# Kernel optimization log

Measured on AMD Instinct MI355X. Metric: run time of the kernel, lower is better.

## Reference

```python
import jax, jax.numpy as jnp
import numpy as np

K = 8  # 2^3 kernel offsets for kernel-size-2, stride-2 transposed conv in 3D (HYPER_CUBE)
HID = 64


def sp_convT(x, W, parent, kofs):
    """Sparse generative transposed conv via kernel map.
    x: [Nin, Cin]; W: [K, Cin, Cout]; parent: [Nout] int; kofs: [Nout] int in [0,K).
    out[j] = x[parent[j]] @ W[kofs[j]].
    """
    xg = x[parent]  # [Nout, Cin] gather
    out = jnp.zeros((parent.shape[0], W.shape[2]), dtype=x.dtype)
    for k in range(K):  # fixed small structural loop over kernel offsets
        out = out + jnp.where((kofs == k)[:, None], xg @ W[k], jnp.zeros((), x.dtype))
    return out


def setup_inputs() -> dict:
    key = jax.random.key(0)
    ks = jax.random.split(key, 12)
    Ns = [5000, 20000, 80000, 320000]
    sc_i = 1.0 / np.sqrt(64)
    inp = {
        'x0': jax.random.normal(ks[0], (Ns[0], 64), jnp.float32),
        'x1': jax.random.normal(ks[1], (Ns[1], 64), jnp.float32),
        'x2': jax.random.normal(ks[2], (Ns[2], 64), jnp.float32),
        'W_i': jax.random.normal(ks[3], (K, 64, 4 * HID), jnp.float32) * sc_i,
        'W_h': jax.random.normal(ks[4], (K, HID, 4 * HID), jnp.float32) * sc_i,
        'W_c': jax.random.normal(ks[5], (K, HID, HID), jnp.float32) * sc_i,
        'parent0': jax.random.randint(ks[6], (Ns[1],), 0, Ns[0], jnp.int32),
        'kofs0': jax.random.randint(ks[7], (Ns[1],), 0, K, jnp.int32),
        'parent1': jax.random.randint(ks[8], (Ns[2],), 0, Ns[1], jnp.int32),
        'kofs1': jax.random.randint(ks[9], (Ns[2],), 0, K, jnp.int32),
        'parent2': jax.random.randint(ks[10], (Ns[3],), 0, Ns[2], jnp.int32),
        'kofs2': jax.random.randint(ks[11], (Ns[3],), 0, K, jnp.int32),
    }
    return inp


def reference(x0, x1, x2, W_i, W_h, W_c, parent0, kofs0, parent1, kofs1, parent2, kofs2):
    xs = [x0, x1, x2]
    parents = [parent0, parent1, parent2]
    kofss = [kofs0, kofs1, kofs2]
    hx = jnp.zeros((x0.shape[0], HID), dtype=x0.dtype)
    cx = jnp.zeros((x0.shape[0], HID), dtype=x0.dtype)
    for t in range(3):  # coder_num timesteps (structural loop)
        p, ko = parents[t], kofss[t]
        cx = sp_convT(cx, W_c, p, ko)                                   # upsample cell state
        gates = sp_convT(hx, W_h, p, ko) + sp_convT(xs[t], W_i, p, ko)  # [Nout, 4*HID]
        in_g, fg, cg, og = jnp.split(gates, 4, axis=1)
        in_g = jax.nn.sigmoid(in_g)
        fg = jax.nn.sigmoid(fg)
        cg = jax.nn.sigmoid(cg)  # NOTE: original uses sigmoid (not tanh) for cell_gate
        og = jax.nn.sigmoid(og)
        cx = fg * cx + in_g * cg
        hx = og * jnp.tanh(cx)
    return hx
```

## Files before the change

### kernel.cpp

```cpp
#include <hip/hip_runtime.h>


#define KNUM 8
#define TM 32
#define STEP_THREADS 256

typedef __attribute__((ext_vector_type(8))) _Float16 f16x8;
typedef __attribute__((ext_vector_type(4))) float f32x4;

__device__ __forceinline__ float fsig(float x) {
  return __builtin_amdgcn_rcpf(1.0f + __expf(-x));
}
__device__ __forceinline__ float ftanh_(float x) {
  float e = __expf(2.0f * x);
  return 1.0f - 2.0f * __builtin_amdgcn_rcpf(e + 1.0f);
}
__device__ __forceinline__ f16x8 to_h8(float4 a, float4 b) {
  f16x8 r;
  r[0] = (_Float16)a.x; r[1] = (_Float16)a.y; r[2] = (_Float16)a.z; r[3] = (_Float16)a.w;
  r[4] = (_Float16)b.x; r[5] = (_Float16)b.y; r[6] = (_Float16)b.z; r[7] = (_Float16)b.w;
  return r;
}

__global__ void prep_w_kernel(const float* __restrict__ Wi, const float* __restrict__ Wh,
                              const float* __restrict__ Wc,
                              _Float16* __restrict__ WgT, _Float16* __restrict__ WcT) {
  int tid = blockIdx.x * blockDim.x + threadIdx.x;
  int stride = gridDim.x * blockDim.x;
  for (int idx = tid; idx < KNUM * 256 * 128; idx += stride) {
    int k  = idx >> 15;
    int co = (idx >> 7) & 255;
    int ci = idx & 127;
    float v = (ci < 64) ? Wh[(k * 64 + ci) * 256 + co]
                        : Wi[(k * 64 + ci - 64) * 256 + co];
    WgT[idx] = (_Float16)v;
  }
  for (int idx = tid; idx < KNUM * 64 * 64; idx += stride) {
    int k  = idx >> 12;
    int co = (idx >> 6) & 63;
    int ci = idx & 63;
    WcT[idx] = (_Float16)Wc[(k * 64 + ci) * 64 + co];
  }
}

__device__ __forceinline__ void seg_select(int b, int& seg, int& rb, int& nb) {
  if (b < 32)       { seg = 0; rb = b;       nb = 32;  }
  else if (b < 160) { seg = 1; rb = b - 32;  nb = 128; }
  else              { seg = 2; rb = b - 160; nb = 352; }
}

__global__ void scatter_all_kernel(const int* __restrict__ k0, const int* __restrict__ p0, int n0,
                                   int2* __restrict__ op0, int cap0,
                                   const int* __restrict__ k1, const int* __restrict__ p1, int n1,
                                   int2* __restrict__ op1, int cap1,
                                   const int* __restrict__ k2, const int* __restrict__ p2, int n2,
                                   int2* __restrict__ op2, int cap2,
                                   int* __restrict__ cursor) {
  int seg, rb, nb;
  seg_select(blockIdx.x, seg, rb, nb);
  const int* kp = seg == 0 ? k0 : seg == 1 ? k1 : k2;
  const int* pp = seg == 0 ? p0 : seg == 1 ? p1 : p2;
  int n   = seg == 0 ? n0 : seg == 1 ? n1 : n2;
  int cap = seg == 0 ? cap0 : seg == 1 ? cap1 : cap2;
  int2* op = seg == 0 ? op0 : seg == 1 ? op1 : op2;
  int* cur = cursor + seg * KNUM;

  __shared__ int h[KNUM], base[KNUM];
  if (threadIdx.x < KNUM) h[threadIdx.x] = 0;
  __syncthreads();
  int chunk = (n + nb - 1) / nb;
  int c0 = rb * chunk;
  int c1 = min(n, c0 + chunk);
  for (int i = c0 + threadIdx.x; i < c1; i += blockDim.x)
    atomicAdd(&h[kp[i]], 1);
  __syncthreads();
  if (threadIdx.x < KNUM) {
    base[threadIdx.x] = h[threadIdx.x] ? atomicAdd(&cur[threadIdx.x], h[threadIdx.x]) : 0;
    h[threadIdx.x] = 0;
  }
  __syncthreads();
  for (int i = c0 + threadIdx.x; i < c1; i += blockDim.x) {
    int k = kp[i];
    int rel = base[k] + atomicAdd(&h[k], 1);
    op[k * cap + rel] = make_int2(i, pp[i]);
  }
}

template <bool FIRST, bool LAST>
__global__ __launch_bounds__(STEP_THREADS)
void lstm_step_kernel(const float* __restrict__ xf32, const _Float16* __restrict__ hc_in,
                      const int2* __restrict__ op, const int* __restrict__ counts, int cap,
                      const _Float16* __restrict__ WgT, const _Float16* __restrict__ WcT,
                      float* __restrict__ out32, _Float16* __restrict__ hc_out, int bpk) {
  __shared__ __align__(16) _Float16 A[TM][136];
  __shared__ __align__(16) _Float16 Cg[TM][72];
  __shared__ int jidx[TM];
  __shared__ __align__(16) char Obuf[9216];
  float (*O32)[68] = (float(*)[68])Obuf;
  _Float16 (*Oh)[72] = (_Float16(*)[72])Obuf;
  _Float16 (*Oc)[72] = (_Float16(*)[72])(Obuf + 32 * 72 * 2);

  const int kb = blockIdx.x & 7;
  const int bi = blockIdx.x >> 3;
  const int cnt = counts[kb];
  const int off = kb * cap;
  const int ntiles = (cnt + TM - 1) / TM;
  if (bi >= ntiles || cnt == 0) return;

  const int tid  = threadIdx.x;
  const int lane = tid & 63;
  const int wcq  = tid >> 6;
  const int l15  = lane & 15;
  const int kg   = lane >> 4;

  f16x8 bg[4][4];
  f16x8 bc[2];
  {
    const _Float16* wgp = WgT + (size_t)kb * (256 * 128);
#pragma unroll
    for (int g = 0; g < 4; ++g)
#pragma unroll
      for (int ks = (FIRST ? 2 : 0); ks < 4; ++ks)
        bg[g][ks] = *(const f16x8*)(wgp + (size_t)(64 * g + 16 * wcq + l15) * 128 + ks * 32 + kg * 8);
    if constexpr (!FIRST) {
      const _Float16* wcp = WcT + (size_t)kb * (64 * 64);
#pragma unroll
      for (int ks = 0; ks < 2; ++ks)
        bc[ks] = *(const f16x8*)(wcp + (size_t)(16 * wcq + l15) * 64 + ks * 32 + kg * 8);
    }
  }

  const int gr  = tid >> 3;
  const int gq8 = tid & 7;

  auto ld_jp = [&](int tt) -> int2 {
    int grow = tt * TM + gr;
    bool v = (tt < ntiles) && (grow < cnt);
    int2 jp = op[off + min(grow, cnt - 1)];
    if (!v) jp.x = -1;
    return jp;
  };

  float4 xA0{}, xA1{}; f16x8 hA{}, cA{}; int jA = -1;
  float4 xB0{}, xB1{}; f16x8 hB{}, cB{}; int jB = -1;
  int2 jpP;

  auto rows_into = [&](int2 jp, float4& rx0, float4& rx1, f16x8& rh, f16x8& rc, int& rj) {
    int p = jp.y;
    const float4* xr = (const float4*)(xf32 + (size_t)p * 64 + gq8 * 8);
    rx0 = xr[0]; rx1 = xr[1];
    if constexpr (!FIRST) {
      const _Float16* hr = hc_in + (size_t)p * 128 + gq8 * 8;
      rh = *(const f16x8*)(hr);
      rc = *(const f16x8*)(hr + 64);
    }
    rj = jp.x;
  };

  rows_into(ld_jp(bi), xA0, xA1, hA, cA, jA);
  rows_into(ld_jp(bi + bpk), xB0, xB1, hB, cB, jB);
  jpP = ld_jp(bi + 2 * bpk);

#define HALF_STEP(TCUR, RX0, RX1, RH, RC, RJ)                                   \
  {                                                                             \
    asm volatile("s_barrier" ::: "memory");         \
    if (gq8 == 0) jidx[gr] = RJ;                                                \
    *(f16x8*)&A[gr][64 + gq8 * 8] = to_h8(RX0, RX1);                            \
    if constexpr (!FIRST) {                                                     \
      *(f16x8*)&A[gr][gq8 * 8]  = RH;                                           \
      *(f16x8*)&Cg[gr][gq8 * 8] = RC;                                           \
    }                                                                           \
    asm volatile("s_waitcnt lgkmcnt(0)\n\ts_barrier" ::: "memory");             \
    rows_into(jpP, RX0, RX1, RH, RC, RJ);         \
    jpP = ld_jp((TCUR) + 3 * bpk);                                              \
    f32x4 aG[2][4];                                                             \
    f32x4 aC[2];                                                                \
    _Pragma("unroll")                                                           \
    for (int rf = 0; rf < 2; ++rf) {                                            \
      _Pragma("unroll")                                                         \
      for (int g = 0; g < 4; ++g) aG[rf][g] = f32x4{0.f, 0.f, 0.f, 0.f};        \
      aC[rf] = f32x4{0.f, 0.f, 0.f, 0.f};                                       \
    }                                                                           \
    _Pragma("unroll")                                                           \
    for (int ks = (FIRST ? 2 : 0); ks < 4; ++ks) {                              \
      _Pragma("unroll")                                                         \
      for (int rf = 0; rf < 2; ++rf) {                                          \
        f16x8 a = *(const f16x8*)&A[16 * rf + l15][ks * 32 + kg * 8];           \
        aG[rf][0] = __builtin_amdgcn_mfma_f32_16x16x32_f16(a, bg[0][ks], aG[rf][0], 0, 0, 0); \
        aG[rf][1] = __builtin_amdgcn_mfma_f32_16x16x32_f16(a, bg[1][ks], aG[rf][1], 0, 0, 0); \
        aG[rf][2] = __builtin_amdgcn_mfma_f32_16x16x32_f16(a, bg[2][ks], aG[rf][2], 0, 0, 0); \
        aG[rf][3] = __builtin_amdgcn_mfma_f32_16x16x32_f16(a, bg[3][ks], aG[rf][3], 0, 0, 0); \
      }                                                                         \
    }                                                                           \
    if constexpr (!FIRST) {                                                     \
      _Pragma("unroll")                                                         \
      for (int ks = 0; ks < 2; ++ks) {                                          \
        _Pragma("unroll")                                                       \
        for (int rf = 0; rf < 2; ++rf) {                                        \
          f16x8 a = *(const f16x8*)&Cg[16 * rf + l15][ks * 32 + kg * 8];        \
          aC[rf] = __builtin_amdgcn_mfma_f32_16x16x32_f16(a, bc[ks], aC[rf], 0, 0, 0); \
        }                                                                       \
      }                                                                         \
    }                                                                           \
                                                  \
    _Pragma("unroll")                                                           \
    for (int rf = 0; rf < 2; ++rf) {                                            \
      _Pragma("unroll")                                                         \
      for (int r = 0; r < 4; ++r) {                                             \
        int row = 16 * rf + kg * 4 + r;           \
        float ing = fsig(aG[rf][0][r]);                                         \
        float fg  = fsig(aG[rf][1][r]);                                         \
        float cgt = fsig(aG[rf][2][r]);       \
        float og  = fsig(aG[rf][3][r]);                                         \
        float cup = FIRST ? 0.0f : aC[rf][r];                                   \
        float cxv = fg * cup + ing * cgt;                                       \
        float hxv = og * ftanh_(cxv);                                           \
        int ch = 16 * wcq + l15;                                                \
        if constexpr (LAST) {                                                   \
          O32[row][ch] = hxv;                                                   \
        } else {                                                                \
          Oh[row][ch] = (_Float16)hxv;                                          \
          Oc[row][ch] = (_Float16)cxv;                                          \
        }                                                                       \
      }                                                                         \
    }                                                                           \
    asm volatile("s_waitcnt lgkmcnt(0)\n\ts_barrier" ::: "memory");             \
                 \
    {                                                                           \
      int srow = tid >> 3, sc = tid & 7;                                        \
      int j = jidx[srow];                                                       \
      if (j >= 0) {                                                             \
        if constexpr (LAST) {                                                   \
          f32x4 v0 = *(const f32x4*)&O32[srow][sc * 8];                         \
          f32x4 v1 = *(const f32x4*)&O32[srow][sc * 8 + 4];                     \
          float* dst = out32 + (size_t)j * 64 + sc * 8;                         \
          *(f32x4*)dst = v0;                                                    \
          *(f32x4*)(dst + 4) = v1;                                              \
        } else {                                                                \
          f16x8 vh = *(const f16x8*)&Oh[srow][sc * 8];                          \
          f16x8 vc = *(const f16x8*)&Oc[srow][sc * 8];                          \
          _Float16* dst = hc_out + (size_t)j * 128 + sc * 8;                    \
          *(f16x8*)dst = vh;                                                    \
          *(f16x8*)(dst + 64) = vc;                                             \
        }                                                                       \
      }                                                                         \
    }                                                                           \
  }

  for (int t = bi; t < ntiles; t += 2 * bpk) {
    HALF_STEP(t, xA0, xA1, hA, cA, jA);
    if (t + bpk < ntiles) {
      HALF_STEP(t + bpk, xB0, xB1, hB, cB, jB);
    }
  }
#undef HALF_STEP
}

static inline int idiv_up(int a, int b) { return (a + b - 1) / b; }

template <bool FIRST, bool LAST>
static void run_step(const float* xf32, const _Float16* hc_in,
                     const int2* op, int nout, const int* counts, int cap,
                     const _Float16* WgT, const _Float16* WcT,
                     float* out32, _Float16* hc_out, hipStream_t stream) {
  int bpk = idiv_up(nout, KNUM * TM);
  if (bpk > 160) bpk = 160;
  if (bpk < 1) bpk = 1;
  lstm_step_kernel<FIRST, LAST><<<dim3(KNUM * bpk), dim3(STEP_THREADS), 0, stream>>>(
      xf32, hc_in, op, counts, cap, WgT, WcT, out32, hc_out, bpk);
}

extern "C" void kernel_launch(void* const* d_in, const int* in_sizes, int n_in,
                              void* d_out, int out_size, void* d_ws, size_t ws_size,
                              hipStream_t stream) {
  const float* x0 = (const float*)d_in[0];
  const float* x1 = (const float*)d_in[1];
  const float* x2 = (const float*)d_in[2];
  const float* Wi = (const float*)d_in[3];
  const float* Wh = (const float*)d_in[4];
  const float* Wc = (const float*)d_in[5];
  const int* parent0 = (const int*)d_in[6];
  const int* kofs0   = (const int*)d_in[7];
  const int* parent1 = (const int*)d_in[8];
  const int* kofs1   = (const int*)d_in[9];
  const int* parent2 = (const int*)d_in[10];
  const int* kofs2   = (const int*)d_in[11];
  const int N1 = in_sizes[6];
  const int N2 = in_sizes[8];
  const int N3 = in_sizes[10];

  const int cap0 = idiv_up(N1, KNUM) + N1 / 32 + 256;
  const int cap1 = idiv_up(N2, KNUM) + N2 / 32 + 256;
  const int cap2 = idiv_up(N3, KNUM) + N3 / 32 + 256;

  char* w = (char*)d_ws;
  auto carve = [&](size_t bytes) {
    char* p = w;
    w += (bytes + 255) & ~(size_t)255;
    return p;
  };
  _Float16* WgT = (_Float16*)carve((size_t)KNUM * 256 * 128 * 2);
  _Float16* WcT = (_Float16*)carve((size_t)KNUM * 64 * 64 * 2);
  int* cursor   = (int*)carve(3 * KNUM * sizeof(int));
  int2* op0     = (int2*)carve((size_t)KNUM * cap0 * sizeof(int2));
  int2* op1     = (int2*)carve((size_t)KNUM * cap1 * sizeof(int2));
  int2* op2     = (int2*)carve((size_t)KNUM * cap2 * sizeof(int2));
  _Float16* hc_a = (_Float16*)carve((size_t)N1 * 128 * 2);
  _Float16* hc_b = (_Float16*)carve((size_t)N2 * 128 * 2);
  (void)ws_size; (void)n_in; (void)out_size;

  hipMemsetAsync(cursor, 0, 3 * KNUM * sizeof(int), stream);
  prep_w_kernel<<<256, 256, 0, stream>>>(Wi, Wh, Wc, WgT, WcT);
  scatter_all_kernel<<<512, 256, 0, stream>>>(kofs0, parent0, N1, op0, cap0,
                                              kofs1, parent1, N2, op1, cap1,
                                              kofs2, parent2, N3, op2, cap2,
                                              cursor);

  run_step<true, false>(x0, nullptr, op0, N1, cursor + 0 * KNUM, cap0,
                        WgT, WcT, nullptr, hc_a, stream);
  run_step<false, false>(x1, hc_a, op1, N2, cursor + 1 * KNUM, cap1,
                         WgT, WcT, nullptr, hc_b, stream);
  run_step<false, true>(x2, hc_b, op2, N3, cursor + 2 * KNUM, cap2,
                        WgT, WcT, (float*)d_out, nullptr, stream);
}
```

Measured before the change: 104.8 us.

## Pack next-step x into fp16 state rows and rewrite scatter with wave ballots

Each LSTM step now reads the next timestep's x row, indexed by the output row, converts it to fp16 and stores it beside h and c in a 192-wide state row. The next step then gathers h, c and x with one contiguous fp16 read per parent instead of a separate fp32 random gather of x. The scatter kernel switches from a strided loop with shared-memory atomics to one element per thread, ranked within each wavefront by ballot and popcount, and launches enough blocks to cover every element. The cost is extra writes and a larger state buffer, plus an extra read of xnext inside each step kernel.

```diff
diff --git a/kernel.cpp b/kernel.cpp
--- a/kernel.cpp
+++ b/kernel.cpp
@@ -43,21 +43,18 @@
   }
 }
 
-__device__ __forceinline__ void seg_select(int b, int& seg, int& rb, int& nb) {
-  if (b < 32)       { seg = 0; rb = b;       nb = 32;  }
-  else if (b < 160) { seg = 1; rb = b - 32;  nb = 128; }
-  else              { seg = 2; rb = b - 160; nb = 352; }
-}
-
 __global__ void scatter_all_kernel(const int* __restrict__ k0, const int* __restrict__ p0, int n0,
                                    int2* __restrict__ op0, int cap0,
                                    const int* __restrict__ k1, const int* __restrict__ p1, int n1,
                                    int2* __restrict__ op1, int cap1,
                                    const int* __restrict__ k2, const int* __restrict__ p2, int n2,
                                    int2* __restrict__ op2, int cap2,
-                                   int* __restrict__ cursor) {
-  int seg, rb, nb;
-  seg_select(blockIdx.x, seg, rb, nb);
+                                   int* __restrict__ cursor, int nb0, int nb1) {
+  int b = blockIdx.x;
+  int seg, rb;
+  if (b < nb0)            { seg = 0; rb = b; }
+  else if (b < nb0 + nb1) { seg = 1; rb = b - nb0; }
+  else                    { seg = 2; rb = b - nb0 - nb1; }
   const int* kp = seg == 0 ? k0 : seg == 1 ? k1 : k2;
   const int* pp = seg == 0 ? p0 : seg == 1 ? p1 : p2;
   int n   = seg == 0 ? n0 : seg == 1 ? n1 : n2;
@@ -65,30 +62,38 @@
   int2* op = seg == 0 ? op0 : seg == 1 ? op1 : op2;
   int* cur = cursor + seg * KNUM;
 
-  __shared__ int h[KNUM], base[KNUM];
-  if (threadIdx.x < KNUM) h[threadIdx.x] = 0;
-  __syncthreads();
-  int chunk = (n + nb - 1) / nb;
-  int c0 = rb * chunk;
-  int c1 = min(n, c0 + chunk);
-  for (int i = c0 + threadIdx.x; i < c1; i += blockDim.x)
-    atomicAdd(&h[kp[i]], 1);
+  const int i = rb * 256 + (int)threadIdx.x;
+  const int lane = threadIdx.x & 63;
+  const int wid  = threadIdx.x >> 6;
+  int myk = (i < n) ? kp[i] : KNUM;
+
+  __shared__ int wcnt[4][KNUM];
+  __shared__ int kbase[KNUM];
+  int myrank = 0;
+#pragma unroll
+  for (int k = 0; k < KNUM; ++k) {
+    unsigned long long m = __ballot(myk == k);
+    if (myk == k) myrank = __popcll(m & ((1ull << lane) - 1ull));
+    if (lane == 0) wcnt[wid][k] = __popcll(m);
+  }
   __syncthreads();
   if (threadIdx.x < KNUM) {
-    base[threadIdx.x] = h[threadIdx.x] ? atomicAdd(&cur[threadIdx.x], h[threadIdx.x]) : 0;
-    h[threadIdx.x] = 0;
+    int tot = wcnt[0][threadIdx.x] + wcnt[1][threadIdx.x] +
+              wcnt[2][threadIdx.x] + wcnt[3][threadIdx.x];
+    kbase[threadIdx.x] = tot ? atomicAdd(&cur[threadIdx.x], tot) : 0;
   }
   __syncthreads();
-  for (int i = c0 + threadIdx.x; i < c1; i += blockDim.x) {
-    int k = kp[i];
-    int rel = base[k] + atomicAdd(&h[k], 1);
-    op[k * cap + rel] = make_int2(i, pp[i]);
+  if (myk < KNUM) {
+    int woff = 0;
+    for (int w = 0; w < wid; ++w) woff += wcnt[w][myk];
+    op[myk * cap + kbase[myk] + woff + myrank] = make_int2(i, pp[i]);
   }
 }
 
 template <bool FIRST, bool LAST>
 __global__ __launch_bounds__(STEP_THREADS)
 void lstm_step_kernel(const float* __restrict__ xf32, const _Float16* __restrict__ hc_in,
+                      const float* __restrict__ xnext,
                       const int2* __restrict__ op, const int* __restrict__ counts, int cap,
                       const _Float16* __restrict__ WgT, const _Float16* __restrict__ WcT,
                       float* __restrict__ out32, _Float16* __restrict__ hc_out, int bpk) {
@@ -132,6 +137,8 @@
 
   const int gr  = tid >> 3;
   const int gq8 = tid & 7;
+  const int srow = tid >> 3;
+  const int sc   = tid & 7;
 
   auto ld_jp = [&](int tt) -> int2 {
     int grow = tt * TM + gr;
@@ -141,37 +148,52 @@
     return jp;
   };
 
-  float4 xA0{}, xA1{}; f16x8 hA{}, cA{}; int jA = -1;
-  float4 xB0{}, xB1{}; f16x8 hB{}, cB{}; int jB = -1;
+  float4 xA0{}, xA1{}; f16x8 hA{}, cA{}, xA{}; int jA = -1;
+  float4 xB0{}, xB1{}; f16x8 hB{}, cB{}, xB{}; int jB = -1;
   int2 jpP;
 
-  auto rows_into = [&](int2 jp, float4& rx0, float4& rx1, f16x8& rh, f16x8& rc, int& rj) {
+  auto rows_into = [&](int2 jp, float4& rx0, float4& rx1,
+                       f16x8& rh, f16x8& rc, f16x8& rx, int& rj) {
     int p = jp.y;
-    const float4* xr = (const float4*)(xf32 + (size_t)p * 64 + gq8 * 8);
-    rx0 = xr[0]; rx1 = xr[1];
-    if constexpr (!FIRST) {
-      const _Float16* hr = hc_in + (size_t)p * 128 + gq8 * 8;
-      rh = *(const f16x8*)(hr);
-      rc = *(const f16x8*)(hr + 64);
+    if constexpr (FIRST) {
+      const float4* xr = (const float4*)(xf32 + (size_t)p * 64 + gq8 * 8);
+      rx0 = xr[0]; rx1 = xr[1];
+    } else {
+      const _Float16* r_ = hc_in + (size_t)p * 192 + gq8 * 8;
+      rh = *(const f16x8*)(r_);
+      rc = *(const f16x8*)(r_ + 64);
+      rx = *(const f16x8*)(r_ + 128);
     }
     rj = jp.x;
   };
 
-  rows_into(ld_jp(bi), xA0, xA1, hA, cA, jA);
-  rows_into(ld_jp(bi + bpk), xB0, xB1, hB, cB, jB);
+  rows_into(ld_jp(bi), xA0, xA1, hA, cA, xA, jA);
+  rows_into(ld_jp(bi + bpk), xB0, xB1, hB, cB, xB, jB);
   jpP = ld_jp(bi + 2 * bpk);
 
-#define HALF_STEP(TCUR, RX0, RX1, RH, RC, RJ)                                   \
+#define HALF_STEP(TCUR, RX0, RX1, RH, RC, RX16, RJ)                             \
   {                                                                             \
     asm volatile("s_barrier" ::: "memory");         \
     if (gq8 == 0) jidx[gr] = RJ;                                                \
-    *(f16x8*)&A[gr][64 + gq8 * 8] = to_h8(RX0, RX1);                            \
-    if constexpr (!FIRST) {                                                     \
+    if constexpr (FIRST) {                                                      \
+      *(f16x8*)&A[gr][64 + gq8 * 8] = to_h8(RX0, RX1);                          \
+    } else {                                                                    \
+      *(f16x8*)&A[gr][64 + gq8 * 8] = RX16;                                     \
       *(f16x8*)&A[gr][gq8 * 8]  = RH;                                           \
       *(f16x8*)&Cg[gr][gq8 * 8] = RC;                                           \
     }                                                                           \
     asm volatile("s_waitcnt lgkmcnt(0)\n\ts_barrier" ::: "memory");             \
-    rows_into(jpP, RX0, RX1, RH, RC, RJ);         \
+                \
+    float4 xn0{}, xn1{};                                                        \
+    int j_st = -1;                                                              \
+    if constexpr (!LAST) {                                                      \
+      j_st = jidx[srow];                                                        \
+      if (j_st >= 0) {                                                          \
+        const float4* xn = (const float4*)(xnext + (size_t)j_st * 64 + sc * 8); \
+        xn0 = xn[0]; xn1 = xn[1];                                               \
+      }                                                                         \
+    }                                                                           \
+    rows_into(jpP, RX0, RX1, RH, RC, RX16, RJ);   \
     jpP = ld_jp((TCUR) + 3 * bpk);                                              \
     f32x4 aG[2][4];                                                             \
     f32x4 aC[2];                                                                \
@@ -226,31 +248,31 @@
     }                                                                           \
     asm volatile("s_waitcnt lgkmcnt(0)\n\ts_barrier" ::: "memory");             \
                  \
-    {                                                                           \
-      int srow = tid >> 3, sc = tid & 7;                                        \
+    if constexpr (LAST) {                                                       \
       int j = jidx[srow];                                                       \
       if (j >= 0) {                                                             \
-        if constexpr (LAST) {                                                   \
-          f32x4 v0 = *(const f32x4*)&O32[srow][sc * 8];                         \
-          f32x4 v1 = *(const f32x4*)&O32[srow][sc * 8 + 4];                     \
-          float* dst = out32 + (size_t)j * 64 + sc * 8;                         \
-          *(f32x4*)dst = v0;                                                    \
-          *(f32x4*)(dst + 4) = v1;                                              \
-        } else {                                                                \
-          f16x8 vh = *(const f16x8*)&Oh[srow][sc * 8];                          \
-          f16x8 vc = *(const f16x8*)&Oc[srow][sc * 8];                          \
-          _Float16* dst = hc_out + (size_t)j * 128 + sc * 8;                    \
-          *(f16x8*)dst = vh;                                                    \
-          *(f16x8*)(dst + 64) = vc;                                             \
-        }                                                                       \
+        f32x4 v0 = *(const f32x4*)&O32[srow][sc * 8];                           \
+        f32x4 v1 = *(const f32x4*)&O32[srow][sc * 8 + 4];                       \
+        float* dst = out32 + (size_t)j * 64 + sc * 8;                           \
+        *(f32x4*)dst = v0;                                                      \
+        *(f32x4*)(dst + 4) = v1;                                                \
+      }                                                                         \
+    } else {                                                                    \
+      if (j_st >= 0) {                                                          \
+        f16x8 vh = *(const f16x8*)&Oh[srow][sc * 8];                            \
+        f16x8 vc = *(const f16x8*)&Oc[srow][sc * 8];                            \
+        _Float16* dst = hc_out + (size_t)j_st * 192 + sc * 8;                   \
+        *(f16x8*)dst = vh;                                                      \
+        *(f16x8*)(dst + 64) = vc;                                               \
+        *(f16x8*)(dst + 128) = to_h8(xn0, xn1);                                 \
       }                                                                         \
     }                                                                           \
   }
 
   for (int t = bi; t < ntiles; t += 2 * bpk) {
-    HALF_STEP(t, xA0, xA1, hA, cA, jA);
+    HALF_STEP(t, xA0, xA1, hA, cA, xA, jA);
     if (t + bpk < ntiles) {
-      HALF_STEP(t + bpk, xB0, xB1, hB, cB, jB);
+      HALF_STEP(t + bpk, xB0, xB1, hB, cB, xB, jB);
     }
   }
 #undef HALF_STEP
@@ -259,7 +281,7 @@
 static inline int idiv_up(int a, int b) { return (a + b - 1) / b; }
 
 template <bool FIRST, bool LAST>
-static void run_step(const float* xf32, const _Float16* hc_in,
+static void run_step(const float* xf32, const _Float16* hc_in, const float* xnext,
                      const int2* op, int nout, const int* counts, int cap,
                      const _Float16* WgT, const _Float16* WcT,
                      float* out32, _Float16* hc_out, hipStream_t stream) {
@@ -267,7 +289,7 @@
   if (bpk > 160) bpk = 160;
   if (bpk < 1) bpk = 1;
   lstm_step_kernel<FIRST, LAST><<<dim3(KNUM * bpk), dim3(STEP_THREADS), 0, stream>>>(
-      xf32, hc_in, op, counts, cap, WgT, WcT, out32, hc_out, bpk);
+      xf32, hc_in, xnext, op, counts, cap, WgT, WcT, out32, hc_out, bpk);
 }
 
 extern "C" void kernel_launch(void* const* d_in, const int* in_sizes, int n_in,
@@ -292,6 +314,7 @@
   const int cap0 = idiv_up(N1, KNUM) + N1 / 32 + 256;
   const int cap1 = idiv_up(N2, KNUM) + N2 / 32 + 256;
   const int cap2 = idiv_up(N3, KNUM) + N3 / 32 + 256;
+  const int nb0 = idiv_up(N1, 256), nb1 = idiv_up(N2, 256), nb2 = idiv_up(N3, 256);
 
   char* w = (char*)d_ws;
   auto carve = [&](size_t bytes) {
@@ -305,21 +328,22 @@
   int2* op0     = (int2*)carve((size_t)KNUM * cap0 * sizeof(int2));
   int2* op1     = (int2*)carve((size_t)KNUM * cap1 * sizeof(int2));
   int2* op2     = (int2*)carve((size_t)KNUM * cap2 * sizeof(int2));
-  _Float16* hc_a = (_Float16*)carve((size_t)N1 * 128 * 2);
-  _Float16* hc_b = (_Float16*)carve((size_t)N2 * 128 * 2);
+  _Float16* hc_a = (_Float16*)carve((size_t)N1 * 192 * 2);
+  _Float16* hc_b = (_Float16*)carve((size_t)N2 * 192 * 2);
   (void)ws_size; (void)n_in; (void)out_size;
 
   hipMemsetAsync(cursor, 0, 3 * KNUM * sizeof(int), stream);
   prep_w_kernel<<<256, 256, 0, stream>>>(Wi, Wh, Wc, WgT, WcT);
-  scatter_all_kernel<<<512, 256, 0, stream>>>(kofs0, parent0, N1, op0, cap0,
-                                              kofs1, parent1, N2, op1, cap1,
-                                              kofs2, parent2, N3, op2, cap2,
-                                              cursor);
-
-  run_step<true, false>(x0, nullptr, op0, N1, cursor + 0 * KNUM, cap0,
+  scatter_all_kernel<<<nb0 + nb1 + nb2, 256, 0, stream>>>(
+      kofs0, parent0, N1, op0, cap0,
+      kofs1, parent1, N2, op1, cap1,
+      kofs2, parent2, N3, op2, cap2,
+      cursor, nb0, nb1);
+
+  run_step<true, false>(x0, nullptr, x1, op0, N1, cursor + 0 * KNUM, cap0,
                         WgT, WcT, nullptr, hc_a, stream);
-  run_step<false, false>(x1, hc_a, op1, N2, cursor + 1 * KNUM, cap1,
+  run_step<false, false>(nullptr, hc_a, x2, op1, N2, cursor + 1 * KNUM, cap1,
                          WgT, WcT, nullptr, hc_b, stream);
-  run_step<false, true>(x2, hc_b, op2, N3, cursor + 2 * KNUM, cap2,
+  run_step<false, true>(nullptr, hc_b, nullptr, op2, N3, cursor + 2 * KNUM, cap2,
                         WgT, WcT, (float*)d_out, nullptr, stream);
 }
```

New measurement: 114.9 us. 1.1x slower.
